# Performance work log

Measured on AMD Instinct MI355X. Metric: run time of the kernel, lower is better.

Reference implementation:

```python
import math
import jax, jax.numpy as jnp
import numpy as np

N_HEADS = 16
D_EMBED = 1024

def setup_inputs() -> dict:
    key = jax.random.key(0)
    ks = jax.random.split(key, 5)
    b, l, d = 2, 2048, D_EMBED
    return {
        "x": jax.random.normal(ks[0], (b, l, d), dtype=jnp.float32),
        "w_in": jax.random.normal(ks[1], (3 * d, d), dtype=jnp.float32) * 0.02,
        "b_in": jax.random.normal(ks[2], (3 * d,), dtype=jnp.float32) * 0.02,
        "w_out": jax.random.normal(ks[3], (d, d), dtype=jnp.float32) * 0.02,
        "b_out": jax.random.normal(ks[4], (d,), dtype=jnp.float32) * 0.02,
    }

def reference(x, w_in, b_in, w_out, b_out):
    b, l, d = x.shape
    h = N_HEADS
    scale = 1.0 / math.sqrt(d // h)
    # in_proj then reshape to heads BEFORE chunking (faithful to source:
    # each head's 3*d_head block is split into q/k/v)
    x_proj = (x @ w_in.T + b_in).reshape(b, l, h, -1)  # (b,l,h,3*dh)
    q, k, v = jnp.split(x_proj, 3, axis=-1)            # each (b,l,h,dh)
    att = jnp.einsum('blhd,bmhd->blmh', q, k) * scale  # (b,l,m,h)
    # causal_mask=False path of the original forward
    att = jax.nn.softmax(att, axis=2)                  # softmax over keys m
    # faithful to source einsum 'blmh, blhd-> blhd' (sums att over m against
    # v indexed by l, exactly as the original code computes)
    opt = jnp.einsum('blmh,blhd->blhd', att, v).reshape(b, l, d)
    return opt @ w_out.T + b_out
```

## Files before the change

### kernel.cpp

```cpp
#include <hip/hip_runtime.h>

typedef unsigned short ushort_t;
typedef __bf16 bf16x8 __attribute__((ext_vector_type(8)));
typedef float f32x4 __attribute__((ext_vector_type(4)));

static __device__ __forceinline__ ushort_t f2bf(float f) {
    __bf16 b = (__bf16)f;
    return __builtin_bit_cast(ushort_t, b);
}

#define GLOAD_LDS16(gptr, lptr)                                                        \
    __builtin_amdgcn_global_load_lds(                                                  \
        (const __attribute__((address_space(1))) void*)(gptr),                         \
        (__attribute__((address_space(3))) void*)(lptr), 16, 0, 0)

#define CFENCE() asm volatile("" ::: "memory")

template <int N> __device__ __forceinline__ void waitcnt_vm() {
    if constexpr (N == 0)      asm volatile("s_waitcnt vmcnt(0)" ::: "memory");
    else if constexpr (N == 2) asm volatile("s_waitcnt vmcnt(2)" ::: "memory");
    else if constexpr (N == 4) asm volatile("s_waitcnt vmcnt(4)" ::: "memory");
    else if constexpr (N == 8) asm volatile("s_waitcnt vmcnt(8)" ::: "memory");
}

template <int BM, int BN, int WGM, int WGN, int THREADS, bool BF16_OUT>
__device__ __forceinline__
void gemm_core(const ushort_t* __restrict__ A, const ushort_t* __restrict__ B,
               const float* __restrict__ bias, void* __restrict__ C,
               const int K, const int N, const int rA, const int rB,
               ushort_t* ls) {
    constexpr int WM = BM / WGM, WN = BN / WGN;
    constexpr int MI = WM / 16, NJ = WN / 16;
    constexpr int LA = (BM * 32) / (8 * THREADS);
    constexpr int LB = (BN * 32) / (8 * THREADS);
    constexpr int L  = LA + LB;
    constexpr int HALF = (BM + BN) * 32;

    const int tid  = threadIdx.x;
    const int lane = tid & 63;
    const int wv   = tid >> 6;
    const int wr   = wv / WGN, wc = wv % WGN;
    const int fr   = lane & 15, fq = lane >> 4;

    f32x4 acc[MI][NJ] = {};

    auto stage = [&](int k0, int buf) {
        #pragma unroll
        for (int q = 0; q < LA; ++q) {
            int c = q * THREADS + tid;
            GLOAD_LDS16(A + (size_t)(rA + (c >> 2)) * K + k0 + (c & 3) * 8,
                        &ls[buf * HALF + c * 8]);
        }
        #pragma unroll
        for (int q = 0; q < LB; ++q) {
            int c = q * THREADS + tid;
            GLOAD_LDS16(B + (size_t)(rB + (c >> 2)) * K + k0 + (c & 3) * 8,
                        &ls[buf * HALF + BM * 32 + c * 8]);
        }
    };

    auto compute = [&](int buf) {
        bf16x8 af[MI], bfv[NJ];
        #pragma unroll
        for (int i = 0; i < MI; ++i)
            af[i] = *(const bf16x8*)&ls[buf * HALF + (wr * WM + i * 16 + fr) * 32 + fq * 8];
        #pragma unroll
        for (int j = 0; j < NJ; ++j)
            bfv[j] = *(const bf16x8*)&ls[buf * HALF + BM * 32 + (wc * WN + j * 16 + fr) * 32 + fq * 8];
        #pragma unroll
        for (int i = 0; i < MI; ++i)
            #pragma unroll
            for (int j = 0; j < NJ; ++j)
                acc[i][j] = __builtin_amdgcn_mfma_f32_16x16x32_bf16(af[i], bfv[j], acc[i][j], 0, 0, 0);
    };

    const int T = K >> 5;
    stage(0, 0);
    stage(32, 1);
    int cur = 0, nxt2 = 2;
    for (int t = 0; t < T - 2; ++t) {
        stage((t + 2) << 5, nxt2);
        waitcnt_vm<2 * L>();
        __builtin_amdgcn_s_barrier(); CFENCE();
        compute(cur);
        CFENCE(); __builtin_amdgcn_s_barrier(); CFENCE();
        cur  = (cur  + 1 == 3) ? 0 : cur  + 1;
        nxt2 = (nxt2 + 1 == 3) ? 0 : nxt2 + 1;
    }
    waitcnt_vm<L>();
    __builtin_amdgcn_s_barrier(); CFENCE();
    compute(cur);
    cur = (cur + 1 == 3) ? 0 : cur + 1;
    CFENCE();
    waitcnt_vm<0>();
    __builtin_amdgcn_s_barrier(); CFENCE();
    compute(cur);

    const int orow0 = rA + wr * WM + fq * 4;
    const int ocol0 = rB + wc * WN + fr;
    #pragma unroll
    for (int i = 0; i < MI; ++i)
        #pragma unroll
        for (int j = 0; j < NJ; ++j) {
            const int col = ocol0 + j * 16;
            const float bv = bias ? bias[col] : 0.f;
            #pragma unroll
            for (int r = 0; r < 4; ++r) {
                const int row = orow0 + i * 16 + r;
                const float v = acc[i][j][r] + bv;
                if constexpr (BF16_OUT)
                    ((ushort_t*)C)[(size_t)row * N + col] = f2bf(v);
                else
                    ((float*)C)[(size_t)row * N + col] = v;
            }
        }
}

__global__ __launch_bounds__(256)
void prep(const float* __restrict__ w_in, const float* __restrict__ b_in,
          const float* __restrict__ w_out, const float* __restrict__ b_out,
          ushort_t* __restrict__ wob, ushort_t* __restrict__ Pt,
          float* __restrict__ bfused) {
    __shared__ ushort_t tile[64][65];
    const int b = blockIdx.x;
    const int t = threadIdx.x;

    if (b < 128) {
        #pragma unroll
        for (int p = 0; p < 8; ++p) {
            int i = b * 2048 + p * 256 + t;
            float4 v = ((const float4*)w_out)[i];
            ushort4 o; o.x = f2bf(v.x); o.y = f2bf(v.y); o.z = f2bf(v.z); o.w = f2bf(v.w);
            ((ushort4*)wob)[i] = o;
        }
    } else if (b < 384) {
        const int g = b - 128;
        const int gx = g & 15, gy = g >> 4;
        #pragma unroll
        for (int p = 0; p < 16; ++p) {
            int e = p * 256 + t;
            int j = e >> 6, c = e & 63;
            tile[j][c] = f2bf(w_in[(size_t)(gx * 192 + 128 + j) * 1024 + gy * 64 + c]);
        }
        __syncthreads();
        #pragma unroll
        for (int p = 0; p < 16; ++p) {
            int e = p * 256 + t;
            int c = e >> 6, j = e & 63;
            Pt[(size_t)(gy * 64 + c) * 1024 + gx * 64 + j] = tile[j][c];
        }
    } else {
        const int w = t >> 6, lane = t & 63;
        const int row = (b - 384) * 4 + w;
        float s = 0.f;
        #pragma unroll
        for (int it = 0; it < 16; ++it) {
            int j = it * 64 + lane;
            int r = (j >> 6) * 192 + 128 + (j & 63);
            s += w_out[(size_t)row * 1024 + j] * b_in[r];
        }
        #pragma unroll
        for (int off = 32; off; off >>= 1) s += __shfl_down(s, off, 64);
        if (lane == 0) bfused[row] = s + b_out[row];
    }
}

__global__ __launch_bounds__(256)
void k2(const ushort_t* __restrict__ wob, const ushort_t* __restrict__ Pt,
        ushort_t* __restrict__ Wfb,
        const float* __restrict__ x, ushort_t* __restrict__ xb) {
    __shared__ alignas(16) ushort_t ls[3 * (64 + 64) * 32];
    const int b = blockIdx.x;
    if (b < 256) {
        const int swz = (b & 7) * 32 + (b >> 3);
        const int by = swz >> 4, bx = swz & 15;
        gemm_core<64, 64, 2, 2, 256, true>(wob, Pt, nullptr, (void*)Wfb, 1024, 1024,
                                           by * 64, bx * 64, ls);
    } else {
        const int g = b - 256;
        const int t = threadIdx.x;
        #pragma unroll
        for (int p = 0; p < 8; ++p) {
            int i = g * 2048 + p * 256 + t;
            float4 v = ((const float4*)x)[i];
            ushort4 o; o.x = f2bf(v.x); o.y = f2bf(v.y); o.z = f2bf(v.z); o.w = f2bf(v.w);
            ((ushort4*)xb)[i] = o;
        }
    }
}

__global__ __launch_bounds__(512)
void k3(const ushort_t* __restrict__ xb, const ushort_t* __restrict__ Wfb,
        const float* __restrict__ bfused, float* __restrict__ out) {
    __shared__ alignas(16) ushort_t ls[3 * (128 + 128) * 32];
    const int b = blockIdx.x;
    const int swz = (b & 7) * 32 + (b >> 3);
    const int by = swz >> 3, bx = swz & 7;
    gemm_core<128, 128, 2, 4, 512, false>(xb, Wfb, bfused, (void*)out, 1024, 1024,
                                          by * 128, bx * 128, ls);
}

extern "C" void kernel_launch(void* const* d_in, const int* in_sizes, int n_in,
                              void* d_out, int out_size, void* d_ws, size_t ws_size,
                              hipStream_t stream) {
    const float* x     = (const float*)d_in[0];
    const float* w_in  = (const float*)d_in[1];
    const float* b_in  = (const float*)d_in[2];
    const float* w_out = (const float*)d_in[3];
    const float* b_out = (const float*)d_in[4];
    float* out = (float*)d_out;

    char* ws = (char*)d_ws;
    ushort_t* xb     = (ushort_t*)(ws);
    ushort_t* wob    = (ushort_t*)(ws + (8u  << 20));
    ushort_t* Pt     = (ushort_t*)(ws + (10u << 20));
    ushort_t* Wfb    = (ushort_t*)(ws + (12u << 20));
    float*    bfused = (float*)   (ws + (14u << 20));

    prep<<<640, 256, 0, stream>>>(w_in, b_in, w_out, b_out, wob, Pt, bfused);
    k2<<<768, 256, 0, stream>>>(wob, Pt, Wfb, x, xb);
    k3<<<256, 512, 0, stream>>>(xb, Wfb, bfused, out);
}
```

Baseline: 36.33 us.

## Double GEMM K-tile to 64 with XOR-swizzled LDS layout

Raises the GEMM K-step from 32 to 64, halving the number of pipeline iterations and barriers. LDS rows are XOR-swizzled so the wider fragment reads avoid bank conflicts, and the async global-to-LDS loads write into the swizzled positions. It also adds an explicit lgkmcnt(0) wait plus a scheduling barrier before the end-of-iteration barrier. In exchange LDS use doubles (96KB for k3), which may lower occupancy.

```diff
diff --git a/kernel.cpp b/kernel.cpp
--- a/kernel.cpp
+++ b/kernel.cpp
@@ -15,26 +15,27 @@
         (__attribute__((address_space(3))) void*)(lptr), 16, 0, 0)
 
 #define CFENCE() asm volatile("" ::: "memory")
+#define LGKM0_SCHED() do { asm volatile("s_waitcnt lgkmcnt(0)" ::: "memory");          \
+                           __builtin_amdgcn_sched_barrier(0); } while (0)
 
 template <int N> __device__ __forceinline__ void waitcnt_vm() {
     if constexpr (N == 0)      asm volatile("s_waitcnt vmcnt(0)" ::: "memory");
-    else if constexpr (N == 2) asm volatile("s_waitcnt vmcnt(2)" ::: "memory");
     else if constexpr (N == 4) asm volatile("s_waitcnt vmcnt(4)" ::: "memory");
     else if constexpr (N == 8) asm volatile("s_waitcnt vmcnt(8)" ::: "memory");
 }
 
 template <int BM, int BN, int WGM, int WGN, int THREADS, bool BF16_OUT>
 __device__ __forceinline__
-void gemm_core(const ushort_t* __restrict__ A, const ushort_t* __restrict__ B,
-               const float* __restrict__ bias, void* __restrict__ C,
-               const int K, const int N, const int rA, const int rB,
-               ushort_t* ls) {
+void gemm_core64(const ushort_t* __restrict__ A, const ushort_t* __restrict__ B,
+                 const float* __restrict__ bias, void* __restrict__ C,
+                 const int K, const int N, const int rA, const int rB,
+                 ushort_t* ls) {
     constexpr int WM = BM / WGM, WN = BN / WGN;
     constexpr int MI = WM / 16, NJ = WN / 16;
-    constexpr int LA = (BM * 32) / (8 * THREADS);
-    constexpr int LB = (BN * 32) / (8 * THREADS);
+    constexpr int LA = (BM * 8) / THREADS;
+    constexpr int LB = (BN * 8) / THREADS;
     constexpr int L  = LA + LB;
-    constexpr int HALF = (BM + BN) * 32;
+    constexpr int HALF = (BM + BN) * 64;
 
     const int tid  = threadIdx.x;
     const int lane = tid & 63;
@@ -48,42 +49,55 @@
         #pragma unroll
         for (int q = 0; q < LA; ++q) {
             int c = q * THREADS + tid;
-            GLOAD_LDS16(A + (size_t)(rA + (c >> 2)) * K + k0 + (c & 3) * 8,
+            int row = c >> 3;
+            int u = (c & 7) ^ (row & 7);
+            GLOAD_LDS16(A + (size_t)(rA + row) * K + k0 + u * 8,
                         &ls[buf * HALF + c * 8]);
         }
         #pragma unroll
         for (int q = 0; q < LB; ++q) {
             int c = q * THREADS + tid;
-            GLOAD_LDS16(B + (size_t)(rB + (c >> 2)) * K + k0 + (c & 3) * 8,
-                        &ls[buf * HALF + BM * 32 + c * 8]);
+            int row = c >> 3;
+            int u = (c & 7) ^ (row & 7);
+            GLOAD_LDS16(B + (size_t)(rB + row) * K + k0 + u * 8,
+                        &ls[buf * HALF + BM * 64 + c * 8]);
         }
     };
 
     auto compute = [&](int buf) {
-        bf16x8 af[MI], bfv[NJ];
-        #pragma unroll
-        for (int i = 0; i < MI; ++i)
-            af[i] = *(const bf16x8*)&ls[buf * HALF + (wr * WM + i * 16 + fr) * 32 + fq * 8];
-        #pragma unroll
-        for (int j = 0; j < NJ; ++j)
-            bfv[j] = *(const bf16x8*)&ls[buf * HALF + BM * 32 + (wc * WN + j * 16 + fr) * 32 + fq * 8];
-        #pragma unroll
-        for (int i = 0; i < MI; ++i)
-            #pragma unroll
-            for (int j = 0; j < NJ; ++j)
-                acc[i][j] = __builtin_amdgcn_mfma_f32_16x16x32_bf16(af[i], bfv[j], acc[i][j], 0, 0, 0);
+        #pragma unroll
+        for (int sub = 0; sub < 2; ++sub) {
+            const int u = sub * 4 + fq;
+            bf16x8 af[MI], bfv[NJ];
+            #pragma unroll
+            for (int i = 0; i < MI; ++i) {
+                const int row = wr * WM + i * 16 + fr;
+                af[i] = *(const bf16x8*)&ls[buf * HALF + row * 64 + (u ^ (row & 7)) * 8];
+            }
+            #pragma unroll
+            for (int j = 0; j < NJ; ++j) {
+                const int row = wc * WN + j * 16 + fr;
+                bfv[j] = *(const bf16x8*)&ls[buf * HALF + BM * 64 + row * 64 + (u ^ (row & 7)) * 8];
+            }
+            #pragma unroll
+            for (int i = 0; i < MI; ++i)
+                #pragma unroll
+                for (int j = 0; j < NJ; ++j)
+                    acc[i][j] = __builtin_amdgcn_mfma_f32_16x16x32_bf16(af[i], bfv[j], acc[i][j], 0, 0, 0);
+        }
     };
 
-    const int T = K >> 5;
+    const int T = K >> 6;
     stage(0, 0);
-    stage(32, 1);
+    stage(64, 1);
     int cur = 0, nxt2 = 2;
     for (int t = 0; t < T - 2; ++t) {
-        stage((t + 2) << 5, nxt2);
+        stage((t + 2) << 6, nxt2);
         waitcnt_vm<2 * L>();
         __builtin_amdgcn_s_barrier(); CFENCE();
         compute(cur);
-        CFENCE(); __builtin_amdgcn_s_barrier(); CFENCE();
+        LGKM0_SCHED();
+        __builtin_amdgcn_s_barrier(); CFENCE();
         cur  = (cur  + 1 == 3) ? 0 : cur  + 1;
         nxt2 = (nxt2 + 1 == 3) ? 0 : nxt2 + 1;
     }
@@ -91,7 +105,7 @@
     __builtin_amdgcn_s_barrier(); CFENCE();
     compute(cur);
     cur = (cur + 1 == 3) ? 0 : cur + 1;
-    CFENCE();
+    LGKM0_SCHED();
     waitcnt_vm<0>();
     __builtin_amdgcn_s_barrier(); CFENCE();
     compute(cur);
@@ -169,13 +183,13 @@
 void k2(const ushort_t* __restrict__ wob, const ushort_t* __restrict__ Pt,
         ushort_t* __restrict__ Wfb,
         const float* __restrict__ x, ushort_t* __restrict__ xb) {
-    __shared__ alignas(16) ushort_t ls[3 * (64 + 64) * 32];
+    __shared__ alignas(16) ushort_t ls[3 * (64 + 64) * 64];
     const int b = blockIdx.x;
     if (b < 256) {
         const int swz = (b & 7) * 32 + (b >> 3);
         const int by = swz >> 4, bx = swz & 15;
-        gemm_core<64, 64, 2, 2, 256, true>(wob, Pt, nullptr, (void*)Wfb, 1024, 1024,
-                                           by * 64, bx * 64, ls);
+        gemm_core64<64, 64, 2, 2, 256, true>(wob, Pt, nullptr, (void*)Wfb, 1024, 1024,
+                                             by * 64, bx * 64, ls);
     } else {
         const int g = b - 256;
         const int t = threadIdx.x;
@@ -192,12 +206,12 @@
 __global__ __launch_bounds__(512)
 void k3(const ushort_t* __restrict__ xb, const ushort_t* __restrict__ Wfb,
         const float* __restrict__ bfused, float* __restrict__ out) {
-    __shared__ alignas(16) ushort_t ls[3 * (128 + 128) * 32];
+    __shared__ alignas(16) ushort_t ls[3 * (128 + 128) * 64];
     const int b = blockIdx.x;
     const int swz = (b & 7) * 32 + (b >> 3);
     const int by = swz >> 3, bx = swz & 7;
-    gemm_core<128, 128, 2, 4, 512, false>(xb, Wfb, bfused, (void*)out, 1024, 1024,
-                                          by * 128, bx * 128, ls);
+    gemm_core64<128, 128, 2, 4, 512, false>(xb, Wfb, bfused, (void*)out, 1024, 1024,
+                                            by * 128, bx * 128, ls);
 }
 
 extern "C" void kernel_launch(void* const* d_in, const int* in_sizes, int n_in,
```

Measured after the change: 33.00 us (median of 2 runs). 1.1x faster.
